# Optimization experiments

Hardware: AMD Instinct MI355X
Metric: run time of the kernel (lower is better)

Reference implementation:

```python
import jax, jax.numpy as jnp
import numpy as np

EPS_MEAN = 1e-10


def setup_inputs() -> dict:
    key = jax.random.key(0)
    ks = jax.random.split(key, 16)
    B, N, F, D = 2, 512, 128, 3
    s = lambda fan_in: 1.0 / np.sqrt(fan_in)
    return {
        "h": jax.random.normal(ks[0], (B, N, F), jnp.float32),
        "coord": jax.random.normal(ks[1], (B, N, D), jnp.float32),
        "mask": jnp.ones((B, N), jnp.float32),
        "edge_w1": jax.random.normal(ks[2], (2 * F + 1, F), jnp.float32) * s(2 * F + 1),
        "edge_b1": jnp.zeros((F,), jnp.float32),
        "edge_w2": jax.random.normal(ks[3], (F, F), jnp.float32) * s(F),
        "edge_b2": jnp.zeros((F,), jnp.float32),
        "node_w1": jax.random.normal(ks[4], (2 * F, F), jnp.float32) * s(2 * F),
        "node_b1": jnp.zeros((F,), jnp.float32),
        "node_w2": jax.random.normal(ks[5], (F, F), jnp.float32) * s(F),
        "node_b2": jnp.zeros((F,), jnp.float32),
        "coord_w1": jax.random.normal(ks[6], (F, F), jnp.float32) * s(F),
        "coord_b1": jnp.zeros((F,), jnp.float32),
        # xavier_uniform with gain=0.001 -> tiny weights
        "coord_w2": jax.random.normal(ks[7], (F, 1), jnp.float32) * 0.001 * s(F),
    }


def reference(h, coord, mask, edge_w1, edge_b1, edge_w2, edge_b2,
              node_w1, node_b1, node_w2, node_b2,
              coord_w1, coord_b1, coord_w2):
    silu = jax.nn.silu
    B, N, F = h.shape
    # mask inputs
    h = h * mask[:, :, None]
    coord = coord * mask[:, :, None]
    mask2d = mask[:, :, None] * mask[:, None, :]            # [B,N,N]

    # coord2radial
    coord_diff = coord[:, :, None] - coord[:, None]          # [B,N,N,3]
    radial = jnp.sum(coord_diff ** 2, axis=-1, keepdims=True)  # [B,N,N,1]
    radial = radial * mask2d[..., None]
    coord_diff = coord_diff * mask2d[..., None]

    # edge model: source[b,i,j]=h[b,j], target[b,i,j]=h[b,i]
    source = jnp.broadcast_to(h[:, None, :, :], (B, N, N, F))
    target = jnp.broadcast_to(h[:, :, None, :], (B, N, N, F))
    edge_in = jnp.concatenate([source, target, radial], axis=-1)  # [B,N,N,2F+1]
    m = silu(edge_in @ edge_w1 + edge_b1)
    m = silu(m @ edge_w2 + edge_b2)                          # [B,N,N,F]
    m = m * mask2d[..., None]

    # coord model
    embed = silu(m @ coord_w1 + coord_b1) @ coord_w2         # [B,N,N,1]
    trans = coord_diff * embed * mask2d[..., None]           # [B,N,N,3]
    denom = jnp.sum(mask2d, axis=2, keepdims=True) + EPS_MEAN  # [B,N,1]
    coord_new = coord + jnp.sum(trans, axis=2) / denom
    coord_new = coord_new * mask[:, :, None]

    # node model
    agg = jnp.sum(m, axis=2)                                 # [B,N,F]
    node_in = jnp.concatenate([h, agg], axis=-1) * mask[:, :, None]
    out = silu(node_in @ node_w1 + node_b1) @ node_w2 + node_b2
    h_new = (h + out) * mask[:, :, None]

    return h_new, coord_new
```

## Files before the change

### kernel.cpp

```cpp
#include <hip/hip_runtime.h>


#define B_ 2
#define N_ 512
#define F_ 128
#define TJ 64
#define MSTRIDE 136

typedef __attribute__((ext_vector_type(8))) short short8;
typedef __attribute__((ext_vector_type(4))) float floatx4;

__device__ __forceinline__ float fsilu(float x) {
    float e = __expf(-x);
    return x * __builtin_amdgcn_rcpf(1.0f + e);
}
__device__ __forceinline__ unsigned pack2(float a, float b) {
    return __builtin_amdgcn_perm(__float_as_uint(b) + 0x8000u,
                                 __float_as_uint(a) + 0x8000u, 0x07060302u);
}

__global__ __launch_bounds__(256) void egcl_prep(
        const float* __restrict__ h, const float* __restrict__ mask,
        const float* __restrict__ ew1, const float* __restrict__ ew2,
        const float* __restrict__ cw1,
        float* __restrict__ Hs, float* __restrict__ Ht,
        unsigned short* __restrict__ W2P, unsigned short* __restrict__ WcP,
        float* __restrict__ msum) {
    __shared__ float sh[8][F_];
    const int blk = blockIdx.x, tid = threadIdx.x;
    if (blk < 128) {
        const int r0 = blk * 8;
        const int col = tid & 127, half = tid >> 7;
#pragma unroll
        for (int rr = 0; rr < 4; ++rr) {
            int row = rr * 2 + half;
            sh[row][col] = h[(r0 + row) * F_ + col] * mask[r0 + row];
        }
        __syncthreads();
        const float* W = ew1 + half * F_ * F_ + col;
        float acc[8] = {0.f, 0.f, 0.f, 0.f, 0.f, 0.f, 0.f, 0.f};
#pragma unroll 8
        for (int k = 0; k < F_; ++k) {
            float w = W[k * F_];
#pragma unroll
            for (int r = 0; r < 8; ++r) acc[r] += sh[r][k] * w;
        }
        float* dst = half ? Ht : Hs;
#pragma unroll
        for (int r = 0; r < 8; ++r) dst[(r0 + r) * F_ + col] = acc[r];
    } else if (blk < 144) {
        const int wsel = (blk - 128) >> 3;
        const int mt = (blk - 128) & 7;
        const float* src = wsel ? cw1 : ew2;
        unsigned short* dst = wsel ? WcP : W2P;
        const int ln = tid & 63, kk = tid >> 6;
        const int qq = ln >> 4, ll = ln & 15;
#pragma unroll
        for (int rep = 0; rep < 2; ++rep) {
            const int krow = kk * 32 + qq * 8 + rep * 4;
            float f0 = src[(krow + 0) * F_ + mt * 16 + ll];
            float f1 = src[(krow + 1) * F_ + mt * 16 + ll];
            float f2 = src[(krow + 2) * F_ + mt * 16 + ll];
            float f3 = src[(krow + 3) * F_ + mt * 16 + ll];
            uint2 u = make_uint2(pack2(f0, f1), pack2(f2, f3));
            *(uint2*)(dst + ((mt * 4 + kk) * 64 + ln) * 8 + rep * 4) = u;
        }
    } else {
        const int bb = blk - 144;
        float v = mask[bb * N_ + tid] + mask[bb * N_ + 256 + tid];
        v += __shfl_xor(v, 1);  v += __shfl_xor(v, 2);
        v += __shfl_xor(v, 4);  v += __shfl_xor(v, 8);
        v += __shfl_xor(v, 16); v += __shfl_xor(v, 32);
        const int wave = tid >> 6, lane = tid & 63;
        if (lane == 0) sh[0][wave] = v;
        __syncthreads();
        if (tid == 0) msum[bb] = sh[0][0] + sh[0][1] + sh[0][2] + sh[0][3];
    }
}

#define L_M1   0
#define L_M    17408
#define L_HB   34816
#define L_W1R  35328
#define L_EMBP 35840
#define L_AGG  36864
#define L_HIN  37376
#define L_AGGT 37888
#define L_TL   38400
#define L_NP   38912
#define L_CSW  39936
#define L_TOTAL 39968

__global__ __launch_bounds__(256, 2) void egcl_main(
        const float* __restrict__ h, const float* __restrict__ coord,
        const float* __restrict__ mask,
        const float* __restrict__ eb1, const float* __restrict__ eb2,
        const float* __restrict__ cb1, const float* __restrict__ cw2,
        const float* __restrict__ nw1, const float* __restrict__ nb1,
        const float* __restrict__ nw2, const float* __restrict__ nb2,
        const float* __restrict__ ew1,
        const float* __restrict__ Hs, const float* __restrict__ Ht,
        const unsigned short* __restrict__ W2P,
        const unsigned short* __restrict__ WcP,
        const float* __restrict__ msum,
        float* __restrict__ out_h, float* __restrict__ out_coord) {
    extern __shared__ char smem[];
    unsigned short* m1s = (unsigned short*)(smem + L_M1);
    unsigned short* ms  = (unsigned short*)(smem + L_M);
    float* HB    = (float*)(smem + L_HB);
    float* W1R   = (float*)(smem + L_W1R);
    float* embp  = (float*)(smem + L_EMBP);
    float* aggs  = (float*)(smem + L_AGG);
    float* hin   = (float*)(smem + L_HIN);
    float* aggt  = (float*)(smem + L_AGGT);
    float* tl    = (float*)(smem + L_TL);
    float* np    = (float*)(smem + L_NP);
    float* csw   = (float*)(smem + L_CSW);

    const int tid  = threadIdx.x;
    const int wave = tid >> 6, lane = tid & 63;
    const int q = lane >> 4, l15 = lane & 15;
    const int wg = wave;
    const int bi = blockIdx.x;
    const int b  = bi >> 9;
    const float mask_i = mask[bi];

    short8 w2f[2][4], wcf[2][4];
#pragma unroll
    for (int s = 0; s < 2; ++s)
#pragma unroll
        for (int kk = 0; kk < 4; ++kk) {
            w2f[s][kk] = *(const short8*)(W2P + (((2 * wg + s) * 4 + kk) * 64 + lane) * 8);
            wcf[s][kk] = *(const short8*)(WcP + (((2 * wg + s) * 4 + kk) * 64 + lane) * 8);
        }
    floatx4 e2b[2], c1b[2], w2c[2];
#pragma unroll
    for (int s = 0; s < 2; ++s) {
        e2b[s] = *(const floatx4*)(eb2 + wg * 32 + s * 16 + q * 4);
        c1b[s] = *(const floatx4*)(cb1 + wg * 32 + s * 16 + q * 4);
        w2c[s] = *(const floatx4*)(cw2 + wg * 32 + s * 16 + q * 4);
    }

    if (tid < F_) {
        HB[tid]  = Ht[bi * F_ + tid] + eb1[tid];
        W1R[tid] = ew1[2 * F_ * F_ + tid];
        hin[tid] = h[bi * F_ + tid] * mask_i;
    }
    const float cmi0 = coord[bi * 3 + 0] * mask_i;
    const float cmi1 = coord[bi * 3 + 1] * mask_i;
    const float cmi2 = coord[bi * 3 + 2] * mask_i;
    __syncthreads();

    const int kseg = tid & 15, jq = tid >> 4;
    float hbk[8], w1k[8];
    {
        const floatx4* hp = (const floatx4*)(HB + kseg * 8);
        const floatx4* wp = (const floatx4*)(W1R + kseg * 8);
        floatx4 a = hp[0], bb2 = hp[1], cc = wp[0], dd = wp[1];
#pragma unroll
        for (int t = 0; t < 4; ++t) {
            hbk[t] = a[t]; hbk[4 + t] = bb2[t];
            w1k[t] = cc[t]; w1k[4 + t] = dd[t];
        }
    }
    floatx4 agg0 = {0.f, 0.f, 0.f, 0.f}, agg1 = {0.f, 0.f, 0.f, 0.f};
    float cs0 = 0.f, cs1 = 0.f, cs2 = 0.f;

    for (int p = 0; p < N_ / TJ; ++p) {
#pragma unroll
        for (int r = 0; r < 4; ++r) {
            int row = jq * 4 + r;
            int jg = b * N_ + p * TJ + row;
            float mj = mask[jg];
            float c0 = coord[jg * 3 + 0] * mj;
            float c1 = coord[jg * 3 + 1] * mj;
            float c2 = coord[jg * 3 + 2] * mj;
            float d0 = cmi0 - c0, d1 = cmi1 - c1, d2 = cmi2 - c2;
            float f2 = mask_i * mj;
            float rad = (d0 * d0 + d1 * d1 + d2 * d2) * f2;
            const floatx4* hsp = (const floatx4*)(Hs + jg * F_ + kseg * 8);
            floatx4 h0 = hsp[0], h1 = hsp[1];
            float x[8];
#pragma unroll
            for (int t = 0; t < 4; ++t) {
                x[t]     = fsilu(h0[t] + hbk[t]     + rad * w1k[t]);
                x[4 + t] = fsilu(h1[t] + hbk[4 + t] + rad * w1k[4 + t]);
            }
            union { short8 s8; unsigned u[4]; } pu;
            pu.u[0] = pack2(x[0], x[1]); pu.u[1] = pack2(x[2], x[3]);
            pu.u[2] = pack2(x[4], x[5]); pu.u[3] = pack2(x[6], x[7]);
            *(short8*)(m1s + row * MSTRIDE + kseg * 8) = pu.s8;
        }
        __syncthreads();
#pragma unroll
        for (int jt = 0; jt < 4; ++jt) {
            const int jrow = jt * 16 + l15;
            const unsigned short* m1r = m1s + jrow * MSTRIDE;
            floatx4 a0 = e2b[0], a1 = e2b[1];
#pragma unroll
            for (int kk = 0; kk < 4; ++kk) {
                short8 bf = *(const short8*)(m1r + kk * 32 + q * 8);
                a0 = __builtin_amdgcn_mfma_f32_16x16x32_bf16(w2f[0][kk], bf, a0, 0, 0, 0);
                a1 = __builtin_amdgcn_mfma_f32_16x16x32_bf16(w2f[1][kk], bf, a1, 0, 0, 0);
            }
            const float f2 = mask_i * mask[b * N_ + p * TJ + jrow];
            float v0[4], v1[4];
#pragma unroll
            for (int rg = 0; rg < 4; ++rg) {
                v0[rg] = fsilu(a0[rg]) * f2;
                v1[rg] = fsilu(a1[rg]) * f2;
                agg0[rg] += v0[rg];
                agg1[rg] += v1[rg];
            }
            unsigned short* mr = ms + jrow * MSTRIDE + wg * 32 + q * 4;
            *(uint2*)(mr)      = make_uint2(pack2(v0[0], v0[1]), pack2(v0[2], v0[3]));
            *(uint2*)(mr + 16) = make_uint2(pack2(v1[0], v1[1]), pack2(v1[2], v1[3]));
        }
        __syncthreads();
#pragma unroll
        for (int jt = 0; jt < 4; ++jt) {
            const int jrow = jt * 16 + l15;
            const unsigned short* mr = ms + jrow * MSTRIDE;
            floatx4 a0 = c1b[0], a1 = c1b[1];
#pragma unroll
            for (int kk = 0; kk < 4; ++kk) {
                short8 bf = *(const short8*)(mr + kk * 32 + q * 8);
                a0 = __builtin_amdgcn_mfma_f32_16x16x32_bf16(wcf[0][kk], bf, a0, 0, 0, 0);
                a1 = __builtin_amdgcn_mfma_f32_16x16x32_bf16(wcf[1][kk], bf, a1, 0, 0, 0);
            }
            float es = 0.f;
#pragma unroll
            for (int rg = 0; rg < 4; ++rg) {
                es += fsilu(a0[rg]) * w2c[0][rg];
                es += fsilu(a1[rg]) * w2c[1][rg];
            }
            es += __shfl_xor(es, 16);
            es += __shfl_xor(es, 32);
            if (q == 0) embp[wg * 64 + jrow] = es;
        }
        __syncthreads();
        if (tid < TJ) {
            float e = embp[tid] + embp[64 + tid] + embp[128 + tid] + embp[192 + tid];
            int jg = b * N_ + p * TJ + tid;
            float mj = mask[jg];
            float c0 = coord[jg * 3 + 0] * mj;
            float c1 = coord[jg * 3 + 1] * mj;
            float c2 = coord[jg * 3 + 2] * mj;
            float f2 = mask_i * mj;
            float w = e * f2 * f2;
            cs0 += (cmi0 - c0) * w;
            cs1 += (cmi1 - c1) * w;
            cs2 += (cmi2 - c2) * w;
        }
    }

#pragma unroll
    for (int rg = 0; rg < 4; ++rg) {
        float v = agg0[rg];
        v += __shfl_xor(v, 1); v += __shfl_xor(v, 2);
        v += __shfl_xor(v, 4); v += __shfl_xor(v, 8);
        agg0[rg] = v;
        float u = agg1[rg];
        u += __shfl_xor(u, 1); u += __shfl_xor(u, 2);
        u += __shfl_xor(u, 4); u += __shfl_xor(u, 8);
        agg1[rg] = u;
    }
    if (l15 == 0) {
        *(floatx4*)(aggs + wg * 32 + q * 4)      = agg0;
        *(floatx4*)(aggs + wg * 32 + 16 + q * 4) = agg1;
    }
    if (wave == 0) {
        cs0 += __shfl_xor(cs0, 1); cs0 += __shfl_xor(cs0, 2);
        cs0 += __shfl_xor(cs0, 4); cs0 += __shfl_xor(cs0, 8);
        cs0 += __shfl_xor(cs0, 16); cs0 += __shfl_xor(cs0, 32);
        cs1 += __shfl_xor(cs1, 1); cs1 += __shfl_xor(cs1, 2);
        cs1 += __shfl_xor(cs1, 4); cs1 += __shfl_xor(cs1, 8);
        cs1 += __shfl_xor(cs1, 16); cs1 += __shfl_xor(cs1, 32);
        cs2 += __shfl_xor(cs2, 1); cs2 += __shfl_xor(cs2, 2);
        cs2 += __shfl_xor(cs2, 4); cs2 += __shfl_xor(cs2, 8);
        cs2 += __shfl_xor(cs2, 16); cs2 += __shfl_xor(cs2, 32);
        if (lane == 0) {
            csw[0] = cs0; csw[1] = cs1; csw[2] = cs2;
        }
    }
    __syncthreads();
    if (tid < F_) aggt[tid] = aggs[tid] * mask_i;
    __syncthreads();
    {
        int half = tid >> 7, col = tid & 127;
        const float* W = nw1 + half * 128 * F_ + col;
        float s = 0.f;
        if (half == 0) {
#pragma unroll 8
            for (int k = 0; k < F_; ++k) s += hin[k] * W[k * F_];
            s *= mask_i;
        } else {
#pragma unroll 8
            for (int k = 0; k < F_; ++k) s += aggt[k] * W[k * F_];
        }
        np[tid] = s;
    }
    __syncthreads();
    if (tid < F_) tl[tid] = fsilu(np[tid] + np[128 + tid] + nb1[tid]);
    __syncthreads();
    if (tid < F_) {
        float s = nb2[tid];
#pragma unroll 8
        for (int k = 0; k < F_; ++k) s += tl[k] * nw2[k * F_ + tid];
        out_h[bi * F_ + tid] = (hin[tid] + s) * mask_i;
    } else if (tid < F_ + 3) {
        int d = tid - F_;
        float denom = mask_i * msum[b] + 1e-10f;
        float cm = (d == 0) ? cmi0 : ((d == 1) ? cmi1 : cmi2);
        out_coord[bi * 3 + d] = (cm + csw[d] * __builtin_amdgcn_rcpf(denom)) * mask_i;
    }
}

extern "C" void kernel_launch(void* const* d_in, const int* in_sizes, int n_in,
                              void* d_out, int out_size, void* d_ws, size_t ws_size,
                              hipStream_t stream) {
    const float* h     = (const float*)d_in[0];
    const float* coord = (const float*)d_in[1];
    const float* mask  = (const float*)d_in[2];
    const float* ew1   = (const float*)d_in[3];
    const float* eb1   = (const float*)d_in[4];
    const float* ew2   = (const float*)d_in[5];
    const float* eb2   = (const float*)d_in[6];
    const float* nw1   = (const float*)d_in[7];
    const float* nb1   = (const float*)d_in[8];
    const float* nw2   = (const float*)d_in[9];
    const float* nb2   = (const float*)d_in[10];
    const float* cw1   = (const float*)d_in[11];
    const float* cb1   = (const float*)d_in[12];
    const float* cw2   = (const float*)d_in[13];

    float* Hs = (float*)d_ws;
    float* Ht = Hs + B_ * N_ * F_;
    unsigned short* W2P = (unsigned short*)(Ht + B_ * N_ * F_);
    unsigned short* WcP = W2P + F_ * F_;
    float* msum = (float*)(WcP + F_ * F_);

    float* out_h = (float*)d_out;
    float* out_coord = out_h + B_ * N_ * F_;

    egcl_prep<<<146, 256, 0, stream>>>(h, mask, ew1, ew2, cw1,
                                       Hs, Ht, W2P, WcP, msum);
    egcl_main<<<B_ * N_, 256, L_TOTAL, stream>>>(
        h, coord, mask, eb1, eb2, cb1, cw2, nw1, nb1, nw2, nb2, ew1,
        Hs, Ht, W2P, WcP, msum, out_h, out_coord);
}
```

Measured before the change: 180.8 us.

## Fold exp2 scaling into weights, use packed silu and hardware bf16 conversion

Pre-scales the edge and coord pre-activations by -log2(e) so that silu needs only a raw exp2, and undoes the scale through the coord output weights and the aggregate. The reciprocal becomes a bit-trick estimate with two Newton steps, written on float2 vectors so packed FP32 math can be used. The manual bf16 rounding is swapped for v_cvt_pk_bf16_f32. Radial and mask products are computed once per tile into LDS by one wave ahead of the next tile, and the tail buffers alias the M1 region to shrink LDS. This cuts VALU work in the silu-heavy inner loops, at the cost of slightly different rounding and an extra dependency on LDS-staged values.

```diff
diff --git a/kernel.cpp b/kernel.cpp
--- a/kernel.cpp
+++ b/kernel.cpp
@@ -7,12 +7,45 @@
 #define TJ 64
 #define MSTRIDE 136
 
+#define CM   (-1.44269504088896340736f)
+#define INVC (-0.69314718055994530942f)
+
 typedef __attribute__((ext_vector_type(8))) short short8;
 typedef __attribute__((ext_vector_type(4))) float floatx4;
+typedef __attribute__((ext_vector_type(2))) float floatx2;
+
+#if defined(__has_builtin)
+#if __has_builtin(__builtin_amdgcn_exp2f)
+#define EXP2F(x) __builtin_amdgcn_exp2f(x)
+#endif
+#endif
+#ifndef EXP2F
+#define EXP2F(x) __expf((x) * 0.69314718055994530942f)
+#endif
 
 __device__ __forceinline__ float fsilu(float x) {
     float e = __expf(-x);
     return x * __builtin_amdgcn_rcpf(1.0f + e);
+}
+__device__ __forceinline__ floatx2 mk2(float a, float b) {
+    floatx2 r; r.x = a; r.y = b; return r;
+}
+__device__ __forceinline__ floatx2 silu2s(floatx2 y) {
+    floatx2 e;
+    e.x = EXP2F(y.x);
+    e.y = EXP2F(y.y);
+    floatx2 d = e + 1.0f;
+    floatx2 r;
+    r.x = __uint_as_float(0x7EF311C3u - __float_as_uint(d.x));
+    r.y = __uint_as_float(0x7EF311C3u - __float_as_uint(d.y));
+    r = r * (2.0f - d * r);
+    r = r * (2.0f - d * r);
+    return y * r;
+}
+__device__ __forceinline__ unsigned cvtpk(float lo, float hi) {
+    unsigned r;
+    asm("v_cvt_pk_bf16_f32 %0, %1, %2" : "=v"(r) : "v"(lo), "v"(hi));
+    return r;
 }
 __device__ __forceinline__ unsigned pack2(float a, float b) {
     return __builtin_amdgcn_perm(__float_as_uint(b) + 0x8000u,
@@ -47,7 +80,7 @@
         }
         float* dst = half ? Ht : Hs;
 #pragma unroll
-        for (int r = 0; r < 8; ++r) dst[(r0 + r) * F_ + col] = acc[r];
+        for (int r = 0; r < 8; ++r) dst[(r0 + r) * F_ + col] = acc[r] * CM;
     } else if (blk < 144) {
         const int wsel = (blk - 128) >> 3;
         const int mt = (blk - 128) & 7;
@@ -83,13 +116,15 @@
 #define L_HB   34816
 #define L_W1R  35328
 #define L_EMBP 35840
-#define L_AGG  36864
-#define L_HIN  37376
-#define L_AGGT 37888
-#define L_TL   38400
-#define L_NP   38912
-#define L_CSW  39936
-#define L_TOTAL 39968
+#define L_HIN  36864
+#define L_RAD  37376
+#define L_F2   37632
+#define L_TOTAL 37888
+#define L_AGG  0
+#define L_AGGT 512
+#define L_TL   1024
+#define L_NP   1536
+#define L_CSW  2560
 
 __global__ __launch_bounds__(256, 2) void egcl_main(
         const float* __restrict__ h, const float* __restrict__ coord,
@@ -110,8 +145,10 @@
     float* HB    = (float*)(smem + L_HB);
     float* W1R   = (float*)(smem + L_W1R);
     float* embp  = (float*)(smem + L_EMBP);
+    float* hin   = (float*)(smem + L_HIN);
+    float* radl  = (float*)(smem + L_RAD);
+    float* f2l   = (float*)(smem + L_F2);
     float* aggs  = (float*)(smem + L_AGG);
-    float* hin   = (float*)(smem + L_HIN);
     float* aggt  = (float*)(smem + L_AGGT);
     float* tl    = (float*)(smem + L_TL);
     float* np    = (float*)(smem + L_NP);
@@ -133,37 +170,57 @@
             w2f[s][kk] = *(const short8*)(W2P + (((2 * wg + s) * 4 + kk) * 64 + lane) * 8);
             wcf[s][kk] = *(const short8*)(WcP + (((2 * wg + s) * 4 + kk) * 64 + lane) * 8);
         }
-    floatx4 e2b[2], c1b[2], w2c[2];
+    floatx4 e2b[2], c1b[2];
+    floatx2 w2c2[4];
 #pragma unroll
     for (int s = 0; s < 2; ++s) {
-        e2b[s] = *(const floatx4*)(eb2 + wg * 32 + s * 16 + q * 4);
-        c1b[s] = *(const floatx4*)(cb1 + wg * 32 + s * 16 + q * 4);
-        w2c[s] = *(const floatx4*)(cw2 + wg * 32 + s * 16 + q * 4);
+        e2b[s] = (*(const floatx4*)(eb2 + wg * 32 + s * 16 + q * 4)) * CM;
+        c1b[s] = (*(const floatx4*)(cb1 + wg * 32 + s * 16 + q * 4)) * CM;
+    }
+    {
+        floatx4 w0 = *(const floatx4*)(cw2 + wg * 32 + 0 * 16 + q * 4);
+        floatx4 w1 = *(const floatx4*)(cw2 + wg * 32 + 1 * 16 + q * 4);
+        w2c2[0] = mk2(w0[0], w0[1]) * INVC;
+        w2c2[1] = mk2(w0[2], w0[3]) * INVC;
+        w2c2[2] = mk2(w1[0], w1[1]) * INVC;
+        w2c2[3] = mk2(w1[2], w1[3]) * INVC;
     }
 
     if (tid < F_) {
-        HB[tid]  = Ht[bi * F_ + tid] + eb1[tid];
-        W1R[tid] = ew1[2 * F_ * F_ + tid];
+        HB[tid]  = Ht[bi * F_ + tid] + CM * eb1[tid];
+        W1R[tid] = CM * ew1[2 * F_ * F_ + tid];
         hin[tid] = h[bi * F_ + tid] * mask_i;
     }
     const float cmi0 = coord[bi * 3 + 0] * mask_i;
     const float cmi1 = coord[bi * 3 + 1] * mask_i;
     const float cmi2 = coord[bi * 3 + 2] * mask_i;
+    if (tid < TJ) {
+        int jg = b * N_ + tid;
+        float mj = mask[jg];
+        float c0 = coord[jg * 3 + 0] * mj;
+        float c1 = coord[jg * 3 + 1] * mj;
+        float c2 = coord[jg * 3 + 2] * mj;
+        float d0 = cmi0 - c0, d1 = cmi1 - c1, d2 = cmi2 - c2;
+        float ff = mask_i * mj;
+        radl[tid] = (d0 * d0 + d1 * d1 + d2 * d2) * ff;
+        f2l[tid]  = ff;
+    }
     __syncthreads();
 
     const int kseg = tid & 15, jq = tid >> 4;
-    float hbk[8], w1k[8];
+    floatx2 hbk2[4], w1k2[4];
     {
         const floatx4* hp = (const floatx4*)(HB + kseg * 8);
         const floatx4* wp = (const floatx4*)(W1R + kseg * 8);
         floatx4 a = hp[0], bb2 = hp[1], cc = wp[0], dd = wp[1];
-#pragma unroll
-        for (int t = 0; t < 4; ++t) {
-            hbk[t] = a[t]; hbk[4 + t] = bb2[t];
-            w1k[t] = cc[t]; w1k[4 + t] = dd[t];
-        }
-    }
-    floatx4 agg0 = {0.f, 0.f, 0.f, 0.f}, agg1 = {0.f, 0.f, 0.f, 0.f};
+        hbk2[0] = mk2(a[0], a[1]);   hbk2[1] = mk2(a[2], a[3]);
+        hbk2[2] = mk2(bb2[0], bb2[1]); hbk2[3] = mk2(bb2[2], bb2[3]);
+        w1k2[0] = mk2(cc[0], cc[1]); w1k2[1] = mk2(cc[2], cc[3]);
+        w1k2[2] = mk2(dd[0], dd[1]); w1k2[3] = mk2(dd[2], dd[3]);
+    }
+    floatx2 ag[4];
+    ag[0] = mk2(0.f, 0.f); ag[1] = mk2(0.f, 0.f);
+    ag[2] = mk2(0.f, 0.f); ag[3] = mk2(0.f, 0.f);
     float cs0 = 0.f, cs1 = 0.f, cs2 = 0.f;
 
     for (int p = 0; p < N_ / TJ; ++p) {
@@ -171,72 +228,76 @@
         for (int r = 0; r < 4; ++r) {
             int row = jq * 4 + r;
             int jg = b * N_ + p * TJ + row;
+            float radm = radl[row];
+            floatx2 rr = mk2(radm, radm);
+            const floatx4* hsp = (const floatx4*)(Hs + jg * F_ + kseg * 8);
+            floatx4 h0 = hsp[0], h1 = hsp[1];
+            floatx2 y0 = mk2(h0[0], h0[1]) + hbk2[0] + rr * w1k2[0];
+            floatx2 y1 = mk2(h0[2], h0[3]) + hbk2[1] + rr * w1k2[1];
+            floatx2 y2 = mk2(h1[0], h1[1]) + hbk2[2] + rr * w1k2[2];
+            floatx2 y3 = mk2(h1[2], h1[3]) + hbk2[3] + rr * w1k2[3];
+            floatx2 x0 = silu2s(y0), x1 = silu2s(y1);
+            floatx2 x2 = silu2s(y2), x3 = silu2s(y3);
+            union { short8 s8; unsigned u[4]; } pu;
+            pu.u[0] = cvtpk(x0.x, x0.y); pu.u[1] = cvtpk(x1.x, x1.y);
+            pu.u[2] = cvtpk(x2.x, x2.y); pu.u[3] = cvtpk(x3.x, x3.y);
+            *(short8*)(m1s + row * MSTRIDE + kseg * 8) = pu.s8;
+        }
+        __syncthreads();
+#pragma unroll
+        for (int jt = 0; jt < 4; ++jt) {
+            const int jrow = jt * 16 + l15;
+            const unsigned short* m1r = m1s + jrow * MSTRIDE;
+            floatx4 a0 = e2b[0], a1 = e2b[1];
+#pragma unroll
+            for (int kk = 0; kk < 4; ++kk) {
+                short8 bf = *(const short8*)(m1r + kk * 32 + q * 8);
+                a0 = __builtin_amdgcn_mfma_f32_16x16x32_bf16(w2f[0][kk], bf, a0, 0, 0, 0);
+                a1 = __builtin_amdgcn_mfma_f32_16x16x32_bf16(w2f[1][kk], bf, a1, 0, 0, 0);
+            }
+            const float f2 = f2l[jrow];
+            floatx2 f22 = mk2(f2, f2);
+            floatx2 p0 = silu2s(mk2(a0[0], a0[1])) * f22;
+            floatx2 p1 = silu2s(mk2(a0[2], a0[3])) * f22;
+            floatx2 p2 = silu2s(mk2(a1[0], a1[1])) * f22;
+            floatx2 p3 = silu2s(mk2(a1[2], a1[3])) * f22;
+            ag[0] += p0; ag[1] += p1; ag[2] += p2; ag[3] += p3;
+            unsigned short* mr = ms + jrow * MSTRIDE + wg * 32 + q * 4;
+            *(uint2*)(mr)      = make_uint2(cvtpk(p0.x, p0.y), cvtpk(p1.x, p1.y));
+            *(uint2*)(mr + 16) = make_uint2(cvtpk(p2.x, p2.y), cvtpk(p3.x, p3.y));
+        }
+        __syncthreads();
+#pragma unroll
+        for (int jt = 0; jt < 4; ++jt) {
+            const int jrow = jt * 16 + l15;
+            const unsigned short* mr = ms + jrow * MSTRIDE;
+            floatx4 a0 = c1b[0], a1 = c1b[1];
+#pragma unroll
+            for (int kk = 0; kk < 4; ++kk) {
+                short8 bf = *(const short8*)(mr + kk * 32 + q * 8);
+                a0 = __builtin_amdgcn_mfma_f32_16x16x32_bf16(wcf[0][kk], bf, a0, 0, 0, 0);
+                a1 = __builtin_amdgcn_mfma_f32_16x16x32_bf16(wcf[1][kk], bf, a1, 0, 0, 0);
+            }
+            floatx2 esv = mk2(0.f, 0.f);
+            esv += silu2s(mk2(a0[0], a0[1])) * w2c2[0];
+            esv += silu2s(mk2(a0[2], a0[3])) * w2c2[1];
+            esv += silu2s(mk2(a1[0], a1[1])) * w2c2[2];
+            esv += silu2s(mk2(a1[2], a1[3])) * w2c2[3];
+            float es = esv.x + esv.y;
+            es += __shfl_xor(es, 16);
+            es += __shfl_xor(es, 32);
+            if (q == 0) embp[wg * 64 + jrow] = es;
+        }
+        if (p < N_ / TJ - 1 && wave == 1) {
+            int jg = b * N_ + (p + 1) * TJ + lane;
             float mj = mask[jg];
             float c0 = coord[jg * 3 + 0] * mj;
             float c1 = coord[jg * 3 + 1] * mj;
             float c2 = coord[jg * 3 + 2] * mj;
             float d0 = cmi0 - c0, d1 = cmi1 - c1, d2 = cmi2 - c2;
-            float f2 = mask_i * mj;
-            float rad = (d0 * d0 + d1 * d1 + d2 * d2) * f2;
-            const floatx4* hsp = (const floatx4*)(Hs + jg * F_ + kseg * 8);
-            floatx4 h0 = hsp[0], h1 = hsp[1];
-            float x[8];
-#pragma unroll
-            for (int t = 0; t < 4; ++t) {
-                x[t]     = fsilu(h0[t] + hbk[t]     + rad * w1k[t]);
-                x[4 + t] = fsilu(h1[t] + hbk[4 + t] + rad * w1k[4 + t]);
-            }
-            union { short8 s8; unsigned u[4]; } pu;
-            pu.u[0] = pack2(x[0], x[1]); pu.u[1] = pack2(x[2], x[3]);
-            pu.u[2] = pack2(x[4], x[5]); pu.u[3] = pack2(x[6], x[7]);
-            *(short8*)(m1s + row * MSTRIDE + kseg * 8) = pu.s8;
-        }
-        __syncthreads();
-#pragma unroll
-        for (int jt = 0; jt < 4; ++jt) {
-            const int jrow = jt * 16 + l15;
-            const unsigned short* m1r = m1s + jrow * MSTRIDE;
-            floatx4 a0 = e2b[0], a1 = e2b[1];
-#pragma unroll
-            for (int kk = 0; kk < 4; ++kk) {
-                short8 bf = *(const short8*)(m1r + kk * 32 + q * 8);
-                a0 = __builtin_amdgcn_mfma_f32_16x16x32_bf16(w2f[0][kk], bf, a0, 0, 0, 0);
-                a1 = __builtin_amdgcn_mfma_f32_16x16x32_bf16(w2f[1][kk], bf, a1, 0, 0, 0);
-            }
-            const float f2 = mask_i * mask[b * N_ + p * TJ + jrow];
-            float v0[4], v1[4];
-#pragma unroll
-            for (int rg = 0; rg < 4; ++rg) {
-                v0[rg] = fsilu(a0[rg]) * f2;
-                v1[rg] = fsilu(a1[rg]) * f2;
-                agg0[rg] += v0[rg];
-                agg1[rg] += v1[rg];
-            }
-            unsigned short* mr = ms + jrow * MSTRIDE + wg * 32 + q * 4;
-            *(uint2*)(mr)      = make_uint2(pack2(v0[0], v0[1]), pack2(v0[2], v0[3]));
-            *(uint2*)(mr + 16) = make_uint2(pack2(v1[0], v1[1]), pack2(v1[2], v1[3]));
-        }
-        __syncthreads();
-#pragma unroll
-        for (int jt = 0; jt < 4; ++jt) {
-            const int jrow = jt * 16 + l15;
-            const unsigned short* mr = ms + jrow * MSTRIDE;
-            floatx4 a0 = c1b[0], a1 = c1b[1];
-#pragma unroll
-            for (int kk = 0; kk < 4; ++kk) {
-                short8 bf = *(const short8*)(mr + kk * 32 + q * 8);
-                a0 = __builtin_amdgcn_mfma_f32_16x16x32_bf16(wcf[0][kk], bf, a0, 0, 0, 0);
-                a1 = __builtin_amdgcn_mfma_f32_16x16x32_bf16(wcf[1][kk], bf, a1, 0, 0, 0);
-            }
-            float es = 0.f;
-#pragma unroll
-            for (int rg = 0; rg < 4; ++rg) {
-                es += fsilu(a0[rg]) * w2c[0][rg];
-                es += fsilu(a1[rg]) * w2c[1][rg];
-            }
-            es += __shfl_xor(es, 16);
-            es += __shfl_xor(es, 32);
-            if (q == 0) embp[wg * 64 + jrow] = es;
+            float ff = mask_i * mj;
+            radl[lane] = (d0 * d0 + d1 * d1 + d2 * d2) * ff;
+            f2l[lane]  = ff;
         }
         __syncthreads();
         if (tid < TJ) {
@@ -254,20 +315,20 @@
         }
     }
 
-#pragma unroll
-    for (int rg = 0; rg < 4; ++rg) {
-        float v = agg0[rg];
+    float agf[8] = {ag[0].x, ag[0].y, ag[1].x, ag[1].y,
+                    ag[2].x, ag[2].y, ag[3].x, ag[3].y};
+#pragma unroll
+    for (int rg = 0; rg < 8; ++rg) {
+        float v = agf[rg];
         v += __shfl_xor(v, 1); v += __shfl_xor(v, 2);
         v += __shfl_xor(v, 4); v += __shfl_xor(v, 8);
-        agg0[rg] = v;
-        float u = agg1[rg];
-        u += __shfl_xor(u, 1); u += __shfl_xor(u, 2);
-        u += __shfl_xor(u, 4); u += __shfl_xor(u, 8);
-        agg1[rg] = u;
+        agf[rg] = v;
     }
     if (l15 == 0) {
-        *(floatx4*)(aggs + wg * 32 + q * 4)      = agg0;
-        *(floatx4*)(aggs + wg * 32 + 16 + q * 4) = agg1;
+        floatx4 o0 = {agf[0], agf[1], agf[2], agf[3]};
+        floatx4 o1 = {agf[4], agf[5], agf[6], agf[7]};
+        *(floatx4*)(aggs + wg * 32 + q * 4)      = o0;
+        *(floatx4*)(aggs + wg * 32 + 16 + q * 4) = o1;
     }
     if (wave == 0) {
         cs0 += __shfl_xor(cs0, 1); cs0 += __shfl_xor(cs0, 2);
@@ -284,7 +345,7 @@
         }
     }
     __syncthreads();
-    if (tid < F_) aggt[tid] = aggs[tid] * mask_i;
+    if (tid < F_) aggt[tid] = aggs[tid] * (mask_i * INVC);
     __syncthreads();
     {
         int half = tid >> 7, col = tid & 127;
```

Result: no change. 177.5 us (median of 2 runs) (-1.8%).
